# Kernel tuning notes

Measured on AMD Instinct MI355X. Metric: run time of the kernel, lower is better.

Reference implementation:

```python
import jax, jax.numpy as jnp
import numpy as np

B, N, F_IN, F_OUT = 8, 2048, 256, 128
ALPHA = 0.2  # LeakyReLU negative slope (smooth=False)
MASK_VAL = -9e15


def setup_inputs() -> dict:
    key = jax.random.key(0)
    k1, k2, k3, k4 = jax.random.split(key, 4)
    h = jax.random.normal(k1, (B, N, F_IN), dtype=jnp.float32)
    adj = jax.random.randint(k2, (B, N, N), 0, 2, dtype=jnp.int32)
    # xavier_uniform with gain=1.414 ~ U(-b, b), b = gain*sqrt(6/(fan_in+fan_out))
    bW = 1.414 * np.sqrt(6.0 / (F_IN + F_OUT))
    W = jax.random.uniform(k3, (F_IN, F_OUT), minval=-bW, maxval=bW, dtype=jnp.float32)
    ba = 1.414 * np.sqrt(6.0 / (2 * F_OUT + 1))
    a = jax.random.uniform(k4, (2 * F_OUT, 1), minval=-ba, maxval=ba, dtype=jnp.float32)
    return {"h": h, "adj": adj, "W": W, "a": a}


def reference(h, adj, W, a):
    Wh = jnp.einsum('bni,io->bno', h, W)              # [B,N,F_OUT]
    fo = Wh.shape[-1]
    a1 = a[:fo, 0]                                    # attends to source i
    a2 = a[fo:, 0]                                    # attends to target j
    # e[b,i,j] = leaky_relu(Wh[b,i]@a1 + Wh[b,j]@a2) — equivalent to the
    # concat([Wh_i, Wh_j]) @ a construction without the O(N^2 * 2F) tensor.
    s1 = Wh @ a1                                      # [B,N]
    s2 = Wh @ a2                                      # [B,N]
    e = jax.nn.leaky_relu(s1[:, :, None] + s2[:, None, :], negative_slope=ALPHA)
    att = jnp.where(adj > 0, e, MASK_VAL)
    att = jax.nn.softmax(att, axis=-1)                # [B,N,N]
    # dropout is identity in eval mode (training=False)
    h_prime = jnp.einsum('bij,bjo->bio', att, Wh)     # [B,N,F_OUT]
    return jax.nn.elu(h_prime)                        # concat=True path
```

## Files before the change

### kernel.cpp

```cpp
#include <hip/hip_runtime.h>
#include <math.h>

#define Bn 8
#define Nn 2048
#define FIn 256
#define FOn 128

typedef __attribute__((ext_vector_type(8))) short short8;
typedef __attribute__((ext_vector_type(4))) float f32x4;
typedef __attribute__((ext_vector_type(4))) unsigned short ushort4v;

__device__ __forceinline__ unsigned short f2bf(float x){
    union { float f; unsigned u; } v; v.f = x;
    unsigned r = v.u + 0x7fffu + ((v.u >> 16) & 1u);
    return (unsigned short)(r >> 16);
}

__global__ void k0_wt(const float* __restrict__ W, unsigned short* __restrict__ WT){
    int o = blockIdx.x, k = threadIdx.x;
    WT[o*FIn + k] = f2bf(W[k*FOn + o]);
}

__global__ __launch_bounds__(256) void k1_gemm(const float* __restrict__ h,
        const unsigned short* __restrict__ WT, const float* __restrict__ a,
        unsigned short* __restrict__ WhT, float* __restrict__ s1, float* __restrict__ s2){
    __shared__ __align__(16) unsigned short tr[128][48];
    __shared__ float ps1[2][32], ps2[2][32];
    int t = threadIdx.x, lane = t & 63, w = t >> 6;
    int rg = w >> 1, ch = w & 1;
    int l16 = lane & 15, khalf = (lane >> 4) * 8;
    long g0 = (long)blockIdx.x * 32;
    int b = (int)(g0 >> 11);
    int i0 = (int)(g0 & 2047);
    long row = g0 + rg*16 + l16;
    f32x4 acc[4];
    #pragma unroll
    for (int nf=0;nf<4;nf++) acc[nf] = (f32x4){0.f,0.f,0.f,0.f};
    #pragma unroll
    for (int ks=0; ks<8; ks++){
        int kb = ks*32 + khalf;
        const float4* hp = (const float4*)(h + row*FIn + kb);
        float4 h0 = hp[0], h1 = hp[1];
        short8 af;
        af[0]=(short)f2bf(h0.x); af[1]=(short)f2bf(h0.y); af[2]=(short)f2bf(h0.z); af[3]=(short)f2bf(h0.w);
        af[4]=(short)f2bf(h1.x); af[5]=(short)f2bf(h1.y); af[6]=(short)f2bf(h1.z); af[7]=(short)f2bf(h1.w);
        #pragma unroll
        for (int nf=0;nf<4;nf++){
            short8 bfv = *(const short8*)(WT + (ch*64 + nf*16 + l16)*FIn + kb);
            acc[nf] = __builtin_amdgcn_mfma_f32_16x16x32_bf16(af, bfv, acc[nf], 0, 0, 0);
        }
    }
    {
        float a1v[4], a2v[4];
        #pragma unroll
        for (int nf=0;nf<4;nf++){
            a1v[nf] = a[ch*64 + nf*16 + l16];
            a2v[nf] = a[FOn + ch*64 + nf*16 + l16];
        }
        #pragma unroll
        for (int r=0;r<4;r++){
            float u1 = 0.f, u2 = 0.f;
            #pragma unroll
            for (int nf=0;nf<4;nf++){ u1 = fmaf(acc[nf][r], a1v[nf], u1); u2 = fmaf(acc[nf][r], a2v[nf], u2); }
            u1 += __shfl_xor(u1, 1); u1 += __shfl_xor(u1, 2); u1 += __shfl_xor(u1, 4); u1 += __shfl_xor(u1, 8);
            u2 += __shfl_xor(u2, 1); u2 += __shfl_xor(u2, 2); u2 += __shfl_xor(u2, 4); u2 += __shfl_xor(u2, 8);
            if (l16 == 0){
                int rloc = rg*16 + ((lane>>4)<<2) + r;
                ps1[ch][rloc] = u1; ps2[ch][rloc] = u2;
            }
        }
    }
    int rbase = rg*16 + ((lane>>4)<<2);
    #pragma unroll
    for (int nf=0;nf<4;nf++)
        #pragma unroll
        for (int r=0;r<4;r++)
            tr[ch*64 + nf*16 + l16][rbase + r] = f2bf(acc[nf][r]);
    __syncthreads();
    if (t < 32){
        s1[g0 + t] = ps1[0][t] + ps1[1][t];
        s2[g0 + t] = ps2[0][t] + ps2[1][t];
    }
    int o = t >> 1, seg = t & 1;
    short8 v0 = *(const short8*)&tr[o][seg*16];
    short8 v1 = *(const short8*)&tr[o][seg*16 + 8];
    unsigned short* dst = WhT + ((long)(b*FOn + o))*Nn + i0 + seg*16;
    *(short8*)(dst)     = v0;
    *(short8*)(dst + 8) = v1;
}

__global__ __launch_bounds__(512) void k3_flash(const int* __restrict__ adj,
        const unsigned short* __restrict__ WhT, const float* __restrict__ s1g,
        const float* __restrict__ s2g, float* __restrict__ out){
    __shared__ __align__(16) unsigned short vt[2][128][72];
    __shared__ __align__(16) unsigned short pt[2][32][72];
    __shared__ float s2t[Nn];
    __shared__ float m_s[32], l_s[32], rs_s[2][32];
    int t = threadIdx.x, lane = t & 63, w = t >> 6;
    int bid = blockIdx.x;
    int b = bid & 7;
    int i0 = (bid >> 3) * 32;
    int q = t >> 4;
    int c = t & 15;
    int rg = w >> 2, cq = w & 3;
    int l16 = lane & 15, khalf = (lane >> 4) * 8;
    if (t < 32){ m_s[t] = -INFINITY; l_s[t] = 0.f; }
    *(float4*)&s2t[t*4] = *(const float4*)(s2g + b*Nn + t*4);
    f32x4 acc[2];
    acc[0] = (f32x4){0.f,0.f,0.f,0.f};
    acc[1] = (f32x4){0.f,0.f,0.f,0.f};
    float s1r = s1g[b*Nn + i0 + q];
    const int* ajbase = adj + ((long)(b*Nn + i0 + q))*Nn + c*4;
    int vrow = t >> 3, vj = (t & 7) * 8;
    const unsigned short* vp0 = WhT + ((long)(b*FOn + vrow))*Nn + vj;
    const unsigned short* vp1 = vp0 + 64*Nn;
    short8 vA0 = *(const short8*)(vp0);
    short8 vA1 = *(const short8*)(vp1);
    int4 ajA = *(const int4*)(ajbase);
    int4 ajB = *(const int4*)(ajbase + 64);
    __syncthreads();

    #pragma unroll 1
    for (int jt = 0; jt < 32; jt++){
        int j0 = jt*64;
        int par = jt & 1;
        *(short8*)&vt[par][vrow][vj]      = vA0;
        *(short8*)&vt[par][vrow + 64][vj] = vA1;
        int jn = (jt < 31) ? j0 + 64 : j0;
        vA0 = *(const short8*)(vp0 + jn);
        vA1 = *(const short8*)(vp1 + jn);
        int4 av = ajA; ajA = ajB;
        int jn2 = (jt < 30) ? j0 + 128 : j0;
        ajB = *(const int4*)(ajbase + jn2);
        float4 s2c = *(const float4*)&s2t[j0 + c*4];
        float sc0 = s1r + s2c.x; sc0 = sc0 > 0.f ? sc0 : 0.2f*sc0; sc0 = av.x > 0 ? sc0 : -9e15f;
        float sc1 = s1r + s2c.y; sc1 = sc1 > 0.f ? sc1 : 0.2f*sc1; sc1 = av.y > 0 ? sc1 : -9e15f;
        float sc2 = s1r + s2c.z; sc2 = sc2 > 0.f ? sc2 : 0.2f*sc2; sc2 = av.z > 0 ? sc2 : -9e15f;
        float sc3 = s1r + s2c.w; sc3 = sc3 > 0.f ? sc3 : 0.2f*sc3; sc3 = av.w > 0 ? sc3 : -9e15f;
        float tm = fmaxf(fmaxf(sc0, sc1), fmaxf(sc2, sc3));
        tm = fmaxf(tm, __shfl_xor(tm, 1));
        tm = fmaxf(tm, __shfl_xor(tm, 2));
        tm = fmaxf(tm, __shfl_xor(tm, 4));
        tm = fmaxf(tm, __shfl_xor(tm, 8));
        float mo = m_s[q];
        float mn = fmaxf(mo, tm);
        float rsc = __expf(mo - mn);
        float p0 = __expf(sc0 - mn), p1 = __expf(sc1 - mn);
        float p2 = __expf(sc2 - mn), p3 = __expf(sc3 - mn);
        float ps = (p0+p1)+(p2+p3);
        ps += __shfl_xor(ps, 1); ps += __shfl_xor(ps, 2);
        ps += __shfl_xor(ps, 4); ps += __shfl_xor(ps, 8);
        if (c == 0){ m_s[q] = mn; l_s[q] = l_s[q]*rsc + ps; rs_s[par][q] = rsc; }
        ushort4v pv;
        pv[0] = f2bf(p0); pv[1] = f2bf(p1); pv[2] = f2bf(p2); pv[3] = f2bf(p3);
        *(ushort4v*)&pt[par][q][c*4] = pv;
        __syncthreads();
        int rb = rg*16 + ((lane>>4)<<2);
        float rv0 = rs_s[par][rb + 0];
        float rv1 = rs_s[par][rb + 1];
        float rv2 = rs_s[par][rb + 2];
        float rv3 = rs_s[par][rb + 3];
        acc[0][0]*=rv0; acc[0][1]*=rv1; acc[0][2]*=rv2; acc[0][3]*=rv3;
        acc[1][0]*=rv0; acc[1][1]*=rv1; acc[1][2]*=rv2; acc[1][3]*=rv3;
        #pragma unroll
        for (int kk=0;kk<2;kk++){
            short8 af = *(const short8*)&pt[par][rg*16 + l16][kk*32 + khalf];
            short8 b0 = *(const short8*)&vt[par][cq*32 + l16][kk*32 + khalf];
            short8 b1 = *(const short8*)&vt[par][cq*32 + 16 + l16][kk*32 + khalf];
            acc[0] = __builtin_amdgcn_mfma_f32_16x16x32_bf16(af, b0, acc[0], 0, 0, 0);
            acc[1] = __builtin_amdgcn_mfma_f32_16x16x32_bf16(af, b1, acc[1], 0, 0, 0);
        }
    }
    int rb = rg*16 + ((lane>>4)<<2);
    #pragma unroll
    for (int reg=0;reg<4;reg++){
        int r = rb + reg;
        float inv = 1.f / l_s[r];
        #pragma unroll
        for (int nf=0;nf<2;nf++){
            float v = acc[nf][reg] * inv;
            v = v > 0.f ? v : (__expf(v) - 1.f);
            out[((long)(b*Nn + i0 + r))*FOn + cq*32 + nf*16 + l16] = v;
        }
    }
}

extern "C" void kernel_launch(void* const* d_in, const int* in_sizes, int n_in,
                              void* d_out, int out_size, void* d_ws, size_t ws_size,
                              hipStream_t stream){
    const float* h  = (const float*)d_in[0];
    const int* adj  = (const int*)d_in[1];
    const float* W  = (const float*)d_in[2];
    const float* a  = (const float*)d_in[3];
    float* out = (float*)d_out;
    char* ws = (char*)d_ws;
    unsigned short* WT  = (unsigned short*)(ws);
    unsigned short* WhT = (unsigned short*)(ws + 65536);
    float* s1           = (float*)(ws + 65536 + 4194304);
    float* s2           = (float*)(ws + 65536 + 4194304 + 65536);

    k0_wt   <<<128, 256, 0, stream>>>(W, WT);
    k1_gemm <<<512, 256, 0, stream>>>(h, WT, a, WhT, s1, s2);
    k3_flash<<<512, 512, 0, stream>>>(adj, WhT, s1, s2, out);
}
```

Before: 229.4 us.

## Replace online softmax with precomputed row max bound and bit-packed adjacency mask

```diff
diff --git a/kernel.cpp b/kernel.cpp
--- a/kernel.cpp
+++ b/kernel.cpp
@@ -89,35 +89,60 @@
     *(short8*)(dst + 8) = v1;
 }
 
+__global__ __launch_bounds__(256) void k2_s2max(const float* __restrict__ s2, float* __restrict__ s2m){
+    __shared__ float red[4];
+    int b = blockIdx.x, t = threadIdx.x;
+    float m = -1e30f;
+    #pragma unroll
+    for (int k=0;k<8;k++) m = fmaxf(m, s2[b*Nn + t + k*256]);
+    m = fmaxf(m, __shfl_xor(m, 1));
+    m = fmaxf(m, __shfl_xor(m, 2));
+    m = fmaxf(m, __shfl_xor(m, 4));
+    m = fmaxf(m, __shfl_xor(m, 8));
+    m = fmaxf(m, __shfl_xor(m, 16));
+    m = fmaxf(m, __shfl_xor(m, 32));
+    if ((t & 63) == 0) red[t >> 6] = m;
+    __syncthreads();
+    if (t == 0) s2m[b] = fmaxf(fmaxf(red[0], red[1]), fmaxf(red[2], red[3]));
+}
+
 __global__ __launch_bounds__(512) void k3_flash(const int* __restrict__ adj,
         const unsigned short* __restrict__ WhT, const float* __restrict__ s1g,
-        const float* __restrict__ s2g, float* __restrict__ out){
+        const float* __restrict__ s2g, const float* __restrict__ s2m,
+        float* __restrict__ out){
     __shared__ __align__(16) unsigned short vt[2][128][72];
     __shared__ __align__(16) unsigned short pt[2][32][72];
+    __shared__ unsigned long long ajw64[1024];
     __shared__ float s2t[Nn];
-    __shared__ float m_s[32], l_s[32], rs_s[2][32];
+    __shared__ float l_s[32];
     int t = threadIdx.x, lane = t & 63, w = t >> 6;
     int bid = blockIdx.x;
     int b = bid & 7;
     int i0 = (bid >> 3) * 32;
-    int q = t >> 4;
-    int c = t & 15;
+    int q = t >> 4, c = t & 15;
     int rg = w >> 2, cq = w & 3;
     int l16 = lane & 15, khalf = (lane >> 4) * 8;
-    if (t < 32){ m_s[t] = -INFINITY; l_s[t] = 0.f; }
     *(float4*)&s2t[t*4] = *(const float4*)(s2g + b*Nn + t*4);
-    f32x4 acc[2];
-    acc[0] = (f32x4){0.f,0.f,0.f,0.f};
-    acc[1] = (f32x4){0.f,0.f,0.f,0.f};
     float s1r = s1g[b*Nn + i0 + q];
-    const int* ajbase = adj + ((long)(b*Nn + i0 + q))*Nn + c*4;
+    float Mx = s1r + s2m[b];
+    Mx = fmaxf(Mx, 0.2f*Mx);
     int vrow = t >> 3, vj = (t & 7) * 8;
     const unsigned short* vp0 = WhT + ((long)(b*FOn + vrow))*Nn + vj;
     const unsigned short* vp1 = vp0 + 64*Nn;
     short8 vA0 = *(const short8*)(vp0);
     short8 vA1 = *(const short8*)(vp1);
-    int4 ajA = *(const int4*)(ajbase);
-    int4 ajB = *(const int4*)(ajbase + 64);
+    const int* ajrow = adj + ((long)(b*Nn + i0))*Nn;
+    #pragma unroll 8
+    for (int i = 0; i < 128; i++){
+        int p = w*128 + i;
+        int av = ajrow[(long)(p >> 5)*Nn + (p & 31)*64 + lane];
+        unsigned long long mask = __ballot(av > 0);
+        if (lane == 0) ajw64[p] = mask;
+    }
+    float lsum = 0.f;
+    f32x4 acc0 = (f32x4){0.f,0.f,0.f,0.f};
+    f32x4 acc1 = (f32x4){0.f,0.f,0.f,0.f};
+    const unsigned* ajw32 = (const unsigned*)ajw64;
     __syncthreads();
 
     #pragma unroll 1
@@ -129,59 +154,48 @@
         int jn = (jt < 31) ? j0 + 64 : j0;
         vA0 = *(const short8*)(vp0 + jn);
         vA1 = *(const short8*)(vp1 + jn);
-        int4 av = ajA; ajA = ajB;
-        int jn2 = (jt < 30) ? j0 + 128 : j0;
-        ajB = *(const int4*)(ajbase + jn2);
+        unsigned word = ajw32[q*64 + jt*2 + (c >> 3)];
+        unsigned nib = (word >> ((c & 7)*4)) & 15u;
         float4 s2c = *(const float4*)&s2t[j0 + c*4];
-        float sc0 = s1r + s2c.x; sc0 = sc0 > 0.f ? sc0 : 0.2f*sc0; sc0 = av.x > 0 ? sc0 : -9e15f;
-        float sc1 = s1r + s2c.y; sc1 = sc1 > 0.f ? sc1 : 0.2f*sc1; sc1 = av.y > 0 ? sc1 : -9e15f;
-        float sc2 = s1r + s2c.z; sc2 = sc2 > 0.f ? sc2 : 0.2f*sc2; sc2 = av.z > 0 ? sc2 : -9e15f;
-        float sc3 = s1r + s2c.w; sc3 = sc3 > 0.f ? sc3 : 0.2f*sc3; sc3 = av.w > 0 ? sc3 : -9e15f;
-        float tm = fmaxf(fmaxf(sc0, sc1), fmaxf(sc2, sc3));
-        tm = fmaxf(tm, __shfl_xor(tm, 1));
-        tm = fmaxf(tm, __shfl_xor(tm, 2));
-        tm = fmaxf(tm, __shfl_xor(tm, 4));
-        tm = fmaxf(tm, __shfl_xor(tm, 8));
-        float mo = m_s[q];
-        float mn = fmaxf(mo, tm);
-        float rsc = __expf(mo - mn);
-        float p0 = __expf(sc0 - mn), p1 = __expf(sc1 - mn);
-        float p2 = __expf(sc2 - mn), p3 = __expf(sc3 - mn);
-        float ps = (p0+p1)+(p2+p3);
-        ps += __shfl_xor(ps, 1); ps += __shfl_xor(ps, 2);
-        ps += __shfl_xor(ps, 4); ps += __shfl_xor(ps, 8);
-        if (c == 0){ m_s[q] = mn; l_s[q] = l_s[q]*rsc + ps; rs_s[par][q] = rsc; }
+        float x0 = s1r + s2c.x; x0 = fmaxf(x0, 0.2f*x0);
+        float x1 = s1r + s2c.y; x1 = fmaxf(x1, 0.2f*x1);
+        float x2 = s1r + s2c.z; x2 = fmaxf(x2, 0.2f*x2);
+        float x3 = s1r + s2c.w; x3 = fmaxf(x3, 0.2f*x3);
+        float p0 = (nib & 1u) ? __expf(x0 - Mx) : 0.f;
+        float p1 = (nib & 2u) ? __expf(x1 - Mx) : 0.f;
+        float p2 = (nib & 4u) ? __expf(x2 - Mx) : 0.f;
+        float p3 = (nib & 8u) ? __expf(x3 - Mx) : 0.f;
+        lsum += (p0 + p1) + (p2 + p3);
         ushort4v pv;
         pv[0] = f2bf(p0); pv[1] = f2bf(p1); pv[2] = f2bf(p2); pv[3] = f2bf(p3);
         *(ushort4v*)&pt[par][q][c*4] = pv;
         __syncthreads();
-        int rb = rg*16 + ((lane>>4)<<2);
-        float rv0 = rs_s[par][rb + 0];
-        float rv1 = rs_s[par][rb + 1];
-        float rv2 = rs_s[par][rb + 2];
-        float rv3 = rs_s[par][rb + 3];
-        acc[0][0]*=rv0; acc[0][1]*=rv1; acc[0][2]*=rv2; acc[0][3]*=rv3;
-        acc[1][0]*=rv0; acc[1][1]*=rv1; acc[1][2]*=rv2; acc[1][3]*=rv3;
         #pragma unroll
         for (int kk=0;kk<2;kk++){
             short8 af = *(const short8*)&pt[par][rg*16 + l16][kk*32 + khalf];
             short8 b0 = *(const short8*)&vt[par][cq*32 + l16][kk*32 + khalf];
             short8 b1 = *(const short8*)&vt[par][cq*32 + 16 + l16][kk*32 + khalf];
-            acc[0] = __builtin_amdgcn_mfma_f32_16x16x32_bf16(af, b0, acc[0], 0, 0, 0);
-            acc[1] = __builtin_amdgcn_mfma_f32_16x16x32_bf16(af, b1, acc[1], 0, 0, 0);
-        }
-    }
+            acc0 = __builtin_amdgcn_mfma_f32_16x16x32_bf16(af, b0, acc0, 0, 0, 0);
+            acc1 = __builtin_amdgcn_mfma_f32_16x16x32_bf16(af, b1, acc1, 0, 0, 0);
+        }
+    }
+    lsum += __shfl_xor(lsum, 1);
+    lsum += __shfl_xor(lsum, 2);
+    lsum += __shfl_xor(lsum, 4);
+    lsum += __shfl_xor(lsum, 8);
+    if (c == 0) l_s[q] = lsum;
+    __syncthreads();
     int rb = rg*16 + ((lane>>4)<<2);
     #pragma unroll
     for (int reg=0;reg<4;reg++){
         int r = rb + reg;
         float inv = 1.f / l_s[r];
-        #pragma unroll
-        for (int nf=0;nf<2;nf++){
-            float v = acc[nf][reg] * inv;
-            v = v > 0.f ? v : (__expf(v) - 1.f);
-            out[((long)(b*Nn + i0 + r))*FOn + cq*32 + nf*16 + l16] = v;
-        }
+        float v0 = acc0[reg] * inv;
+        float v1 = acc1[reg] * inv;
+        v0 = v0 > 0.f ? v0 : (__expf(v0) - 1.f);
+        v1 = v1 > 0.f ? v1 : (__expf(v1) - 1.f);
+        out[((long)(b*Nn + i0 + r))*FOn + cq*32 + l16]      = v0;
+        out[((long)(b*Nn + i0 + r))*FOn + cq*32 + 16 + l16] = v1;
     }
 }
 
@@ -198,8 +212,10 @@
     unsigned short* WhT = (unsigned short*)(ws + 65536);
     float* s1           = (float*)(ws + 65536 + 4194304);
     float* s2           = (float*)(ws + 65536 + 4194304 + 65536);
-
-    k0_wt   <<<128, 256, 0, stream>>>(W, WT);
-    k1_gemm <<<512, 256, 0, stream>>>(h, WT, a, WhT, s1, s2);
-    k3_flash<<<512, 512, 0, stream>>>(adj, WhT, s1, s2, out);
-}
+    float* s2m          = (float*)(ws + 65536 + 4194304 + 131072);
+
+    k0_wt    <<<128, 256, 0, stream>>>(W, WT);
+    k1_gemm  <<<512, 256, 0, stream>>>(h, WT, a, WhT, s1, s2);
+    k2_s2max <<<Bn,  256, 0, stream>>>(s2, s2m);
+    k3_flash <<<512, 512, 0, stream>>>(adj, WhT, s1, s2, s2m, out);
+}
```

Result: slower. 292.3 us (+27.4%).
